# Performance work log

Measured on AMD Instinct MI355X. Metric: run time of the kernel, lower is better.

## Reference

```python
import jax, jax.numpy as jnp
import numpy as np

B, S, DIN = 4, 2048, 1024
H, D = 16, 64  # num_head, per-head dim_out


def _xavier(key, shape):
    fan_in, fan_out = shape[0], shape[1]
    limit = float(np.sqrt(6.0 / (fan_in + fan_out)))
    return jax.random.uniform(key, shape, jnp.float32, -limit, limit)


def setup_inputs() -> dict:
    key = jax.random.key(0)
    k_x, k_q, k_k, k_v, k_o = jax.random.split(key, 5)
    inputs = jax.random.normal(k_x, (B, S, DIN), jnp.float32)
    # weights stored as [in, out] (transpose of torch Linear.weight); bias zeros
    return {
        "inputs": inputs,
        "wq": _xavier(k_q, (DIN, H * D)), "bq": jnp.zeros((H * D,), jnp.float32),
        "wk": _xavier(k_k, (DIN, H * D)), "bk": jnp.zeros((H * D,), jnp.float32),
        "wv": _xavier(k_v, (DIN, H * D)), "bv": jnp.zeros((H * D,), jnp.float32),
        "wo": _xavier(k_o, (H * D, D)),  "bo": jnp.zeros((D,), jnp.float32),
    }


def reference(inputs, wq, bq, wk, bk, wv, bv, wo, bo):
    b, s, _ = inputs.shape
    q = (inputs @ wq + bq).reshape(b, s, H, D).transpose(0, 2, 1, 3)  # bhsd
    k = (inputs @ wk + bk).reshape(b, s, H, D).transpose(0, 2, 1, 3)
    v = (inputs @ wv + bv).reshape(b, s, H, D).transpose(0, 2, 1, 3)
    scores = jnp.einsum('bhsd,bhSd->bhsS', q, k) / jnp.sqrt(jnp.float32(D))
    p = jax.nn.softmax(scores, axis=-1)
    o = jnp.einsum('bhsS,bhSd->bhsd', p, v)
    o = o.transpose(0, 2, 1, 3).reshape(b, s, H * D)
    return o @ wo + bo  # [b, s, D]
```

## Files before the change

### kernel.cpp

```cpp
#include <hip/hip_runtime.h>

typedef __attribute__((ext_vector_type(8))) __bf16 bf16x8;
typedef __attribute__((ext_vector_type(4))) float f32x4;

#define NB   4
#define NS   2048
#define NDIN 1024
#define NH   16
#define ND   64
#define NHD  1024
#define NM   (NB * NS)

__device__ __forceinline__ float bf2f(unsigned short u) {
    unsigned int x = ((unsigned int)u) << 16;
    return __builtin_bit_cast(float, x);
}
__device__ __forceinline__ unsigned short f2bf(float f) {
    unsigned int u = __builtin_bit_cast(unsigned int, f);
    u += 0x7fff + ((u >> 16) & 1);
    return (unsigned short)(u >> 16);
}
__device__ __forceinline__ unsigned int cvt_pk_bf16(float lo, float hi) {
    unsigned int r;
    asm("v_cvt_pk_bf16_f32 %0, %1, %2" : "=v"(r) : "v"(lo), "v"(hi));
    return r;
}
__device__ __forceinline__ void gload16(const unsigned short* g, unsigned short* l) {
    __builtin_amdgcn_global_load_lds((const __attribute__((address_space(1))) unsigned int*)g,
                                     (__attribute__((address_space(3))) unsigned int*)l, 16, 0, 0);
}

__global__ __launch_bounds__(256) void cvt_x(const float* __restrict__ src,
                                             unsigned short* __restrict__ dst) {
    int i = blockIdx.x * 256 + threadIdx.x;
    float4 a = ((const float4*)src)[i * 2];
    float4 b = ((const float4*)src)[i * 2 + 1];
    union { uint4 u; unsigned short s[8]; } o;
    o.s[0] = f2bf(a.x); o.s[1] = f2bf(a.y); o.s[2] = f2bf(a.z); o.s[3] = f2bf(a.w);
    o.s[4] = f2bf(b.x); o.s[5] = f2bf(b.y); o.s[6] = f2bf(b.z); o.s[7] = f2bf(b.w);
    *(uint4*)(dst + (size_t)i * 8) = o.u;
}

__global__ void transpose_cvt3(const float* __restrict__ wq, const float* __restrict__ wk,
                               const float* __restrict__ wv, unsigned short* __restrict__ dst_all) {
    __shared__ unsigned short t[32][33];
    const float* src = blockIdx.z == 0 ? wq : blockIdx.z == 1 ? wk : wv;
    unsigned short* dst = dst_all + (size_t)blockIdx.z * 1024 * 1024;
    int k0 = blockIdx.x * 32, n0 = blockIdx.y * 32;
    int tx = threadIdx.x, ty = threadIdx.y;
#pragma unroll
    for (int i = 0; i < 32; i += 8)
        t[ty + i][tx] = f2bf(src[(size_t)(k0 + ty + i) * 1024 + (n0 + tx)]);
    __syncthreads();
#pragma unroll
    for (int i = 0; i < 32; i += 8)
        dst[(size_t)(n0 + ty + i) * 1024 + (k0 + tx)] = t[tx][ty + i];
}

__global__ void transpose_cvt(const float* __restrict__ src,
                              unsigned short* __restrict__ dst, int K, int N) {
    __shared__ unsigned short t[32][33];
    int k0 = blockIdx.x * 32, n0 = blockIdx.y * 32;
    int tx = threadIdx.x, ty = threadIdx.y;
#pragma unroll
    for (int i = 0; i < 32; i += 8)
        t[ty + i][tx] = f2bf(src[(size_t)(k0 + ty + i) * N + (n0 + tx)]);
    __syncthreads();
#pragma unroll
    for (int i = 0; i < 32; i += 8)
        dst[(size_t)(n0 + ty + i) * K + (k0 + tx)] = t[tx][ty + i];
}

__global__ __launch_bounds__(256) void gemm_qkv(
    const unsigned short* __restrict__ X, const unsigned short* __restrict__ Wt,
    const float* __restrict__ bq, const float* __restrict__ bk,
    const float* __restrict__ bv,
    unsigned short* __restrict__ Q, unsigned short* __restrict__ K,
    unsigned short* __restrict__ V) {
    __shared__ unsigned short smem[128 * 128];
    unsigned short (*Al)[32] = (unsigned short (*)[32])smem;
    unsigned short (*Bl)[32] = (unsigned short (*)[32])(smem + 128 * 32);
    unsigned short (*Cl)[128] = (unsigned short (*)[128])smem;

    int lin = blockIdx.x;
    int xcd = lin & 7, ii = lin >> 3;
    int mt = xcd * 8 + (ii & 7);
    int nt = ii >> 3;
    int mb = mt * 128, nb = nt * 128;

    int tid = threadIdx.x;
    int wid = tid >> 6, lane = tid & 63, quad = lane >> 4, l16 = lane & 15;
    int wm = (wid & 1) * 64, wn = (wid >> 1) * 64;

    int srow = 16 * wid + (lane >> 2);
    int scol = (lane & 3) * 8;
    const unsigned short* pa0 = X + (size_t)(mb + srow) * NDIN + scol;
    const unsigned short* pa1 = pa0 + (size_t)64 * NDIN;
    const unsigned short* pb0 = Wt + (size_t)(nb + srow) * NDIN + scol;
    const unsigned short* pb1 = pb0 + (size_t)64 * NDIN;
    unsigned short* la = smem + wid * 512;
    unsigned short* lb = smem + 128 * 32 + wid * 512;

    f32x4 acc[4][4];
#pragma unroll
    for (int i = 0; i < 4; i++)
#pragma unroll
        for (int j = 0; j < 4; j++) acc[i][j] = (f32x4){0.f, 0.f, 0.f, 0.f};

    for (int k0 = 0; k0 < NDIN; k0 += 32) {
        gload16(pa0, la);
        gload16(pa1, la + 2048);
        gload16(pb0, lb);
        gload16(pb1, lb + 2048);
        pa0 += 32; pa1 += 32; pb0 += 32; pb1 += 32;
        __syncthreads();
        bf16x8 af[4], bfr[4];
#pragma unroll
        for (int i = 0; i < 4; i++)
            af[i] = *(const bf16x8*)(&Al[wm + i * 16 + l16][quad * 8]);
#pragma unroll
        for (int j = 0; j < 4; j++)
            bfr[j] = *(const bf16x8*)(&Bl[wn + j * 16 + l16][quad * 8]);
#pragma unroll
        for (int i = 0; i < 4; i++)
#pragma unroll
            for (int j = 0; j < 4; j++)
                acc[i][j] = __builtin_amdgcn_mfma_f32_16x16x32_bf16(af[i], bfr[j], acc[i][j], 0, 0, 0);
        __syncthreads();
    }

    int wsel = nb >> 10;
    const float* bias = (wsel == 0) ? bq : (wsel == 1) ? bk : bv;
    unsigned short* dstp = (wsel == 0) ? Q : (wsel == 1) ? K : V;
#pragma unroll
    for (int i = 0; i < 4; i++)
#pragma unroll
        for (int j = 0; j < 4; j++) {
            int nl = wn + j * 16 + l16;
            float bias_v = bias[(nb & 1023) + nl];
#pragma unroll
            for (int r = 0; r < 4; r++) {
                int ml = wm + i * 16 + quad * 4 + r;
                int pc = ((nl >> 3) ^ (ml & 15));
                Cl[ml][(pc << 3) | (nl & 7)] = f2bf(acc[i][j][r] + bias_v);
            }
        }
    __syncthreads();
    {
        int hl = tid >> 7, sl = tid & 127;
        int h = ((nb & 1023) >> 6) + hl;
        int m = mb + sl, b = m >> 11, sidx = m & 2047;
        unsigned short* orow = dstp + ((size_t)((b * NH + h) * NS + sidx)) * ND;
#pragma unroll
        for (int c = 0; c < 8; c++) {
            int pc = ((hl * 8 + c) ^ (sl & 15));
            *(uint4*)(orow + c * 8) = *(const uint4*)(&Cl[sl][pc << 3]);
        }
    }
}

__global__ __launch_bounds__(256) void attn(
    const unsigned short* __restrict__ Q, const unsigned short* __restrict__ K,
    const unsigned short* __restrict__ V, unsigned short* __restrict__ Obuf) {
    __shared__ unsigned short Kl[2][64][64];
    __shared__ unsigned short Vt[2][64][64];

    int lin = blockIdx.x;
    int xcd = lin & 7, idx = lin >> 3;
    int bh = ((idx >> 4) << 3) | xcd;
    int qt = idx & 15;

    size_t base = (size_t)bh * NS * ND;
    int tid = threadIdx.x, wid = tid >> 6, lane = tid & 63;
    int quad = lane >> 4, l16 = lane & 15;
    int lx = l16 & 7;
    int q0 = qt * 128 + wid * 32;

    bf16x8 qa[2][2];
#pragma unroll
    for (int s = 0; s < 2; s++)
#pragma unroll
        for (int f = 0; f < 2; f++) {
            union { uint4 u; unsigned short sv[8]; } in_, out_;
            in_.u = *(const uint4*)(Q + base + (size_t)(q0 + s * 16 + l16) * ND + f * 32 + quad * 8);
#pragma unroll
            for (int j = 0; j < 8; j++) out_.sv[j] = f2bf(bf2f(in_.sv[j]) * 0.125f);
            qa[s][f] = __builtin_bit_cast(bf16x8, out_.u);
        }

    float lrow[2] = {0.f, 0.f};
    f32x4 o[2][4];
#pragma unroll
    for (int s = 0; s < 2; s++)
#pragma unroll
        for (int t = 0; t < 4; t++) o[s][t] = (f32x4){0.f, 0.f, 0.f, 0.f};

    int c0 = tid, c1 = tid + 256;
    int kr0w = c0 >> 3, kc0 = c0 & 7, kg0c = kc0 ^ (kr0w & 7);
    int kr1w = c1 >> 3, kc1 = c1 & 7, kg1c = kc1 ^ (kr1w & 7);
    const unsigned short* kp0 = K + base + (size_t)kr0w * ND + kc0 * 8;
    const unsigned short* kp1 = K + base + (size_t)kr1w * ND + kc1 * 8;
    int p = tid & 31, dqA = tid >> 5, dqB = dqA + 8;
    int cp = ((p >> 4) << 2) | ((p >> 1) & 3);
    int ps = (((p >> 3) & 1) << 2) | ((p & 1) << 1);
    int cb = cp ^ ((dqA & 1) << 2);
    const unsigned short* vg = V + base + (size_t)(2 * p) * ND + dqA * 4;

    uint4 k0r, k1r;
    uint2 va0, va1, va2, va3;

    auto writeKV = [&](int buf) {
        *(uint4*)(&Kl[buf][kr0w][kg0c * 8]) = k0r;
        *(uint4*)(&Kl[buf][kr1w][kg1c * 8]) = k1r;
        unsigned short* vt = &Vt[buf][0][0];
        unsigned int w0 = __builtin_amdgcn_perm(va1.x, va0.x, 0x05040100u);
        unsigned int w1 = __builtin_amdgcn_perm(va1.x, va0.x, 0x07060302u);
        unsigned int w2 = __builtin_amdgcn_perm(va1.y, va0.y, 0x05040100u);
        unsigned int w3 = __builtin_amdgcn_perm(va1.y, va0.y, 0x07060302u);
        *(unsigned int*)(vt + (dqA * 4 + 0) * 64 + ((cb ^ 0) << 3) + ps) = w0;
        *(unsigned int*)(vt + (dqA * 4 + 1) * 64 + ((cb ^ 1) << 3) + ps) = w1;
        *(unsigned int*)(vt + (dqA * 4 + 2) * 64 + ((cb ^ 2) << 3) + ps) = w2;
        *(unsigned int*)(vt + (dqA * 4 + 3) * 64 + ((cb ^ 3) << 3) + ps) = w3;
        unsigned int x0 = __builtin_amdgcn_perm(va3.x, va2.x, 0x05040100u);
        unsigned int x1 = __builtin_amdgcn_perm(va3.x, va2.x, 0x07060302u);
        unsigned int x2 = __builtin_amdgcn_perm(va3.y, va2.y, 0x05040100u);
        unsigned int x3 = __builtin_amdgcn_perm(va3.y, va2.y, 0x07060302u);
        *(unsigned int*)(vt + (dqB * 4 + 0) * 64 + ((cb ^ 0) << 3) + ps) = x0;
        *(unsigned int*)(vt + (dqB * 4 + 1) * 64 + ((cb ^ 1) << 3) + ps) = x1;
        *(unsigned int*)(vt + (dqB * 4 + 2) * 64 + ((cb ^ 2) << 3) + ps) = x2;
        *(unsigned int*)(vt + (dqB * 4 + 3) * 64 + ((cb ^ 3) << 3) + ps) = x3;
    };

    k0r = *(const uint4*)kp0;
    k1r = *(const uint4*)kp1;
    va0 = *(const uint2*)(vg);
    va1 = *(const uint2*)(vg + ND);
    va2 = *(const uint2*)(vg + 32);
    va3 = *(const uint2*)(vg + ND + 32);
    writeKV(0);
    __syncthreads();

    int cur = 0;
    for (int kc = 0; kc < NS; kc += 64) {
        bool more = (kc + 64 < NS);
        if (more) {
            kp0 += 64 * ND; kp1 += 64 * ND; vg += 64 * ND;
            k0r = *(const uint4*)kp0;
            k1r = *(const uint4*)kp1;
            va0 = *(const uint2*)(vg);
            va1 = *(const uint2*)(vg + ND);
            va2 = *(const uint2*)(vg + 32);
            va3 = *(const uint2*)(vg + ND + 32);
        }

        const unsigned short (*Kc)[64] = Kl[cur];
        const unsigned short (*Vc)[64] = Vt[cur];

        f32x4 st[2][4];
        __builtin_amdgcn_s_setprio(1);
#pragma unroll
        for (int sub = 0; sub < 4; sub++) {
            bf16x8 kb0 = *(const bf16x8*)(&Kc[sub * 16 + l16][((quad ^ lx) << 3)]);
            bf16x8 kb1 = *(const bf16x8*)(&Kc[sub * 16 + l16][(((4 + quad) ^ lx) << 3)]);
#pragma unroll
            for (int s = 0; s < 2; s++) {
                f32x4 c = (f32x4){0.f, 0.f, 0.f, 0.f};
                c = __builtin_amdgcn_mfma_f32_16x16x32_bf16(kb0, qa[s][0], c, 0, 0, 0);
                c = __builtin_amdgcn_mfma_f32_16x16x32_bf16(kb1, qa[s][1], c, 0, 0, 0);
                st[s][sub] = c;
            }
        }
        __builtin_amdgcn_s_setprio(0);

        bf16x8 pb[2][2];
#pragma unroll
        for (int s = 0; s < 2; s++) {
            float sum = 0.f;
#pragma unroll
            for (int sub = 0; sub < 4; sub++)
#pragma unroll
                for (int r = 0; r < 4; r++) {
                    float pv = __expf(st[s][sub][r]);
                    st[s][sub][r] = pv;
                    sum += pv;
                }
            lrow[s] += sum;
            unsigned int a0 = cvt_pk_bf16(st[s][0][0], st[s][0][1]);
            unsigned int a1 = cvt_pk_bf16(st[s][0][2], st[s][0][3]);
            unsigned int a2 = cvt_pk_bf16(st[s][1][0], st[s][1][1]);
            unsigned int a3 = cvt_pk_bf16(st[s][1][2], st[s][1][3]);
            pb[s][0] = __builtin_bit_cast(bf16x8, (uint4){a0, a1, a2, a3});
            unsigned int b0 = cvt_pk_bf16(st[s][2][0], st[s][2][1]);
            unsigned int b1 = cvt_pk_bf16(st[s][2][2], st[s][2][3]);
            unsigned int b2 = cvt_pk_bf16(st[s][3][0], st[s][3][1]);
            unsigned int b3 = cvt_pk_bf16(st[s][3][2], st[s][3][3]);
            pb[s][1] = __builtin_bit_cast(bf16x8, (uint4){b0, b1, b2, b3});
        }

        __builtin_amdgcn_s_setprio(1);
#pragma unroll
        for (int t = 0; t < 4; t++) {
            bf16x8 vb0 = *(const bf16x8*)(&Vc[t * 16 + l16][((quad ^ lx) << 3)]);
            bf16x8 vb1 = *(const bf16x8*)(&Vc[t * 16 + l16][(((4 + quad) ^ lx) << 3)]);
#pragma unroll
            for (int s = 0; s < 2; s++) {
                o[s][t] = __builtin_amdgcn_mfma_f32_16x16x32_bf16(vb0, pb[s][0], o[s][t], 0, 0, 0);
                o[s][t] = __builtin_amdgcn_mfma_f32_16x16x32_bf16(vb1, pb[s][1], o[s][t], 0, 0, 0);
            }
        }
        __builtin_amdgcn_s_setprio(0);

        if (more) {
            int nxt = cur ^ 1;
            writeKV(nxt);
            __syncthreads();
            cur = nxt;
        }
    }

    int b = bh >> 4, h = bh & 15;
#pragma unroll
    for (int s = 0; s < 2; s++) {
        float ls = lrow[s];
        ls += __shfl_xor(ls, 16, 64);
        ls += __shfl_xor(ls, 32, 64);
        float inv = 1.0f / ls;
        int q = q0 + s * 16 + l16;
#pragma unroll
        for (int t = 0; t < 4; t++) {
            uint2 w;
            w.x = cvt_pk_bf16(o[s][t][0] * inv, o[s][t][1] * inv);
            w.y = cvt_pk_bf16(o[s][t][2] * inv, o[s][t][3] * inv);
            *(uint2*)(Obuf + (size_t)(b * NS + q) * NHD + h * ND + t * 16 + quad * 4) = w;
        }
    }
}

__global__ __launch_bounds__(256) void out_proj(
    const unsigned short* __restrict__ Obuf, const unsigned short* __restrict__ WoT,
    const float* __restrict__ bo, float* __restrict__ Out) {
    __shared__ float red[4][16][64];
    int m0 = blockIdx.x * 16;
    int tid = threadIdx.x, wid = tid >> 6, lane = tid & 63;
    int quad = lane >> 4, l16 = lane & 15;
    f32x4 acc[4];
#pragma unroll
    for (int t = 0; t < 4; t++) acc[t] = (f32x4){0.f, 0.f, 0.f, 0.f};
    int kb = wid * 256;
    for (int k0 = kb; k0 < kb + 256; k0 += 32) {
        bf16x8 a = *(const bf16x8*)(Obuf + (size_t)(m0 + l16) * NHD + k0 + quad * 8);
#pragma unroll
        for (int t = 0; t < 4; t++) {
            bf16x8 b = *(const bf16x8*)(WoT + (size_t)(t * 16 + l16) * NHD + k0 + quad * 8);
            acc[t] = __builtin_amdgcn_mfma_f32_16x16x32_bf16(a, b, acc[t], 0, 0, 0);
        }
    }
#pragma unroll
    for (int t = 0; t < 4; t++)
#pragma unroll
        for (int r = 0; r < 4; r++) red[wid][t * 4 + r][lane] = acc[t][r];
    __syncthreads();
    if (tid < 64) {
        int q2 = tid >> 4, s16 = tid & 15;
#pragma unroll
        for (int t = 0; t < 4; t++) {
            int n = t * 16 + s16;
            float bb = bo[n];
#pragma unroll
            for (int r = 0; r < 4; r++) {
                int idx = t * 4 + r;
                float v = red[0][idx][tid] + red[1][idx][tid] + red[2][idx][tid] + red[3][idx][tid];
                int m = m0 + q2 * 4 + r;
                Out[(size_t)m * ND + n] = v + bb;
            }
        }
    }
}

extern "C" void kernel_launch(void* const* d_in, const int* in_sizes, int n_in,
                              void* d_out, int out_size, void* d_ws, size_t ws_size,
                              hipStream_t stream) {
    const float* X  = (const float*)d_in[0];
    const float* wq = (const float*)d_in[1];
    const float* bq = (const float*)d_in[2];
    const float* wk = (const float*)d_in[3];
    const float* bk = (const float*)d_in[4];
    const float* wv = (const float*)d_in[5];
    const float* bv = (const float*)d_in[6];
    const float* wo = (const float*)d_in[7];
    const float* bo = (const float*)d_in[8];
    float* Out = (float*)d_out;

    char* w = (char*)d_ws;
    unsigned short* Wt  = (unsigned short*)w; w += (size_t)3072 * 1024 * 2;
    unsigned short* WoT = (unsigned short*)w; w += (size_t)64 * 1024 * 2;
    unsigned short* Xb  = (unsigned short*)w; w += (size_t)NM * NDIN * 2;
    unsigned short* Qb  = (unsigned short*)w; w += (size_t)NM * NHD * 2;
    unsigned short* Kb  = (unsigned short*)w; w += (size_t)NM * NHD * 2;
    unsigned short* Vb  = (unsigned short*)w; w += (size_t)NM * NHD * 2;
    unsigned short* Ob  = (unsigned short*)w; w += (size_t)NM * NHD * 2;

    cvt_x<<<NM * NDIN / (256 * 8), 256, 0, stream>>>(X, Xb);

    dim3 tb(32, 8);
    transpose_cvt3<<<dim3(32, 32, 3), tb, 0, stream>>>(wq, wk, wv, Wt);
    transpose_cvt<<<dim3(32, 2), tb, 0, stream>>>(wo, WoT, 1024, 64);

    gemm_qkv<<<1536, 256, 0, stream>>>(Xb, Wt, bq, bk, bv, Qb, Kb, Vb);
    attn<<<1024, 256, 0, stream>>>(Qb, Kb, Vb, Ob);
    out_proj<<<512, 256, 0, stream>>>(Ob, WoT, bo, Out);
}
```

Baseline: 277.4 us.

## Double-buffer QKV GEMM LDS tiles and split attention across eight waves

```diff
diff --git a/kernel.cpp b/kernel.cpp
--- a/kernel.cpp
+++ b/kernel.cpp
@@ -77,10 +77,7 @@
     const float* __restrict__ bv,
     unsigned short* __restrict__ Q, unsigned short* __restrict__ K,
     unsigned short* __restrict__ V) {
-    __shared__ unsigned short smem[128 * 128];
-    unsigned short (*Al)[32] = (unsigned short (*)[32])smem;
-    unsigned short (*Bl)[32] = (unsigned short (*)[32])(smem + 128 * 32);
-    unsigned short (*Cl)[128] = (unsigned short (*)[128])smem;
+    __shared__ unsigned short smem[16384];
 
     int lin = blockIdx.x;
     int xcd = lin & 7, ii = lin >> 3;
@@ -98,37 +95,47 @@
     const unsigned short* pa1 = pa0 + (size_t)64 * NDIN;
     const unsigned short* pb0 = Wt + (size_t)(nb + srow) * NDIN + scol;
     const unsigned short* pb1 = pb0 + (size_t)64 * NDIN;
-    unsigned short* la = smem + wid * 512;
-    unsigned short* lb = smem + 128 * 32 + wid * 512;
-
-    f32x4 acc[4][4];
-#pragma unroll
-    for (int i = 0; i < 4; i++)
-#pragma unroll
-        for (int j = 0; j < 4; j++) acc[i][j] = (f32x4){0.f, 0.f, 0.f, 0.f};
-
-    for (int k0 = 0; k0 < NDIN; k0 += 32) {
+
+    auto stage = [&](int buf) {
+        unsigned short* la = smem + buf * 8192 + wid * 512;
+        unsigned short* lb = smem + buf * 8192 + 4096 + wid * 512;
         gload16(pa0, la);
         gload16(pa1, la + 2048);
         gload16(pb0, lb);
         gload16(pb1, lb + 2048);
         pa0 += 32; pa1 += 32; pb0 += 32; pb1 += 32;
-        __syncthreads();
+    };
+
+    f32x4 acc[4][4];
+#pragma unroll
+    for (int i = 0; i < 4; i++)
+#pragma unroll
+        for (int j = 0; j < 4; j++) acc[i][j] = (f32x4){0.f, 0.f, 0.f, 0.f};
+
+    stage(0);
+    __syncthreads();
+    int cur = 0;
+    for (int k0 = 0; k0 < NDIN; k0 += 32) {
+        if (k0 + 32 < NDIN) stage(cur ^ 1);
+        const unsigned short* Ab = smem + cur * 8192;
+        const unsigned short* Bb = Ab + 4096;
         bf16x8 af[4], bfr[4];
 #pragma unroll
         for (int i = 0; i < 4; i++)
-            af[i] = *(const bf16x8*)(&Al[wm + i * 16 + l16][quad * 8]);
+            af[i] = *(const bf16x8*)(Ab + (wm + i * 16 + l16) * 32 + quad * 8);
 #pragma unroll
         for (int j = 0; j < 4; j++)
-            bfr[j] = *(const bf16x8*)(&Bl[wn + j * 16 + l16][quad * 8]);
+            bfr[j] = *(const bf16x8*)(Bb + (wn + j * 16 + l16) * 32 + quad * 8);
 #pragma unroll
         for (int i = 0; i < 4; i++)
 #pragma unroll
             for (int j = 0; j < 4; j++)
                 acc[i][j] = __builtin_amdgcn_mfma_f32_16x16x32_bf16(af[i], bfr[j], acc[i][j], 0, 0, 0);
         __syncthreads();
-    }
-
+        cur ^= 1;
+    }
+
+    unsigned short (*Cl)[128] = (unsigned short (*)[128])smem;
     int wsel = nb >> 10;
     const float* bias = (wsel == 0) ? bq : (wsel == 1) ? bk : bv;
     unsigned short* dstp = (wsel == 0) ? Q : (wsel == 1) ? K : V;
@@ -159,7 +166,7 @@
     }
 }
 
-__global__ __launch_bounds__(256) void attn(
+__global__ __launch_bounds__(512) void attn(
     const unsigned short* __restrict__ Q, const unsigned short* __restrict__ K,
     const unsigned short* __restrict__ V, unsigned short* __restrict__ Obuf) {
     __shared__ unsigned short Kl[2][64][64];
@@ -174,69 +181,50 @@
     int tid = threadIdx.x, wid = tid >> 6, lane = tid & 63;
     int quad = lane >> 4, l16 = lane & 15;
     int lx = l16 & 7;
-    int q0 = qt * 128 + wid * 32;
-
-    bf16x8 qa[2][2];
-#pragma unroll
-    for (int s = 0; s < 2; s++)
-#pragma unroll
-        for (int f = 0; f < 2; f++) {
-            union { uint4 u; unsigned short sv[8]; } in_, out_;
-            in_.u = *(const uint4*)(Q + base + (size_t)(q0 + s * 16 + l16) * ND + f * 32 + quad * 8);
-#pragma unroll
-            for (int j = 0; j < 8; j++) out_.sv[j] = f2bf(bf2f(in_.sv[j]) * 0.125f);
-            qa[s][f] = __builtin_bit_cast(bf16x8, out_.u);
-        }
-
-    float lrow[2] = {0.f, 0.f};
-    f32x4 o[2][4];
-#pragma unroll
-    for (int s = 0; s < 2; s++)
-#pragma unroll
-        for (int t = 0; t < 4; t++) o[s][t] = (f32x4){0.f, 0.f, 0.f, 0.f};
-
-    int c0 = tid, c1 = tid + 256;
-    int kr0w = c0 >> 3, kc0 = c0 & 7, kg0c = kc0 ^ (kr0w & 7);
-    int kr1w = c1 >> 3, kc1 = c1 & 7, kg1c = kc1 ^ (kr1w & 7);
-    const unsigned short* kp0 = K + base + (size_t)kr0w * ND + kc0 * 8;
-    const unsigned short* kp1 = K + base + (size_t)kr1w * ND + kc1 * 8;
-    int p = tid & 31, dqA = tid >> 5, dqB = dqA + 8;
+    int q0 = qt * 128 + wid * 16;
+
+    bf16x8 qa[2];
+#pragma unroll
+    for (int f = 0; f < 2; f++) {
+        union { uint4 u; unsigned short sv[8]; } in_, out_;
+        in_.u = *(const uint4*)(Q + base + (size_t)(q0 + l16) * ND + f * 32 + quad * 8);
+#pragma unroll
+        for (int j = 0; j < 8; j++) out_.sv[j] = f2bf(bf2f(in_.sv[j]) * 0.125f);
+        qa[f] = __builtin_bit_cast(bf16x8, out_.u);
+    }
+
+    float lrow = 0.f;
+    f32x4 o[4];
+#pragma unroll
+    for (int t = 0; t < 4; t++) o[t] = (f32x4){0.f, 0.f, 0.f, 0.f};
+
+    int krow = tid >> 3, kch = tid & 7, kgc = kch ^ (krow & 7);
+    const unsigned short* kp = K + base + (size_t)krow * ND + kch * 8;
+    int p = tid & 31, dq = tid >> 5;
     int cp = ((p >> 4) << 2) | ((p >> 1) & 3);
     int ps = (((p >> 3) & 1) << 2) | ((p & 1) << 1);
-    int cb = cp ^ ((dqA & 1) << 2);
-    const unsigned short* vg = V + base + (size_t)(2 * p) * ND + dqA * 4;
-
-    uint4 k0r, k1r;
-    uint2 va0, va1, va2, va3;
+    int cb = cp ^ ((dq & 1) << 2);
+    const unsigned short* vg = V + base + (size_t)(2 * p) * ND + dq * 4;
+
+    uint4 kreg;
+    uint2 va0, va1;
 
     auto writeKV = [&](int buf) {
-        *(uint4*)(&Kl[buf][kr0w][kg0c * 8]) = k0r;
-        *(uint4*)(&Kl[buf][kr1w][kg1c * 8]) = k1r;
+        *(uint4*)(&Kl[buf][krow][kgc * 8]) = kreg;
         unsigned short* vt = &Vt[buf][0][0];
         unsigned int w0 = __builtin_amdgcn_perm(va1.x, va0.x, 0x05040100u);
         unsigned int w1 = __builtin_amdgcn_perm(va1.x, va0.x, 0x07060302u);
         unsigned int w2 = __builtin_amdgcn_perm(va1.y, va0.y, 0x05040100u);
         unsigned int w3 = __builtin_amdgcn_perm(va1.y, va0.y, 0x07060302u);
-        *(unsigned int*)(vt + (dqA * 4 + 0) * 64 + ((cb ^ 0) << 3) + ps) = w0;
-        *(unsigned int*)(vt + (dqA * 4 + 1) * 64 + ((cb ^ 1) << 3) + ps) = w1;
-        *(unsigned int*)(vt + (dqA * 4 + 2) * 64 + ((cb ^ 2) << 3) + ps) = w2;
-        *(unsigned int*)(vt + (dqA * 4 + 3) * 64 + ((cb ^ 3) << 3) + ps) = w3;
-        unsigned int x0 = __builtin_amdgcn_perm(va3.x, va2.x, 0x05040100u);
-        unsigned int x1 = __builtin_amdgcn_perm(va3.x, va2.x, 0x07060302u);
-        unsigned int x2 = __builtin_amdgcn_perm(va3.y, va2.y, 0x05040100u);
-        unsigned int x3 = __builtin_amdgcn_perm(va3.y, va2.y, 0x07060302u);
-        *(unsigned int*)(vt + (dqB * 4 + 0) * 64 + ((cb ^ 0) << 3) + ps) = x0;
-        *(unsigned int*)(vt + (dqB * 4 + 1) * 64 + ((cb ^ 1) << 3) + ps) = x1;
-        *(unsigned int*)(vt + (dqB * 4 + 2) * 64 + ((cb ^ 2) << 3) + ps) = x2;
-        *(unsigned int*)(vt + (dqB * 4 + 3) * 64 + ((cb ^ 3) << 3) + ps) = x3;
+        *(unsigned int*)(vt + (dq * 4 + 0) * 64 + ((cb ^ 0) << 3) + ps) = w0;
+        *(unsigned int*)(vt + (dq * 4 + 1) * 64 + ((cb ^ 1) << 3) + ps) = w1;
+        *(unsigned int*)(vt + (dq * 4 + 2) * 64 + ((cb ^ 2) << 3) + ps) = w2;
+        *(unsigned int*)(vt + (dq * 4 + 3) * 64 + ((cb ^ 3) << 3) + ps) = w3;
     };
 
-    k0r = *(const uint4*)kp0;
-    k1r = *(const uint4*)kp1;
+    kreg = *(const uint4*)kp;
     va0 = *(const uint2*)(vg);
     va1 = *(const uint2*)(vg + ND);
-    va2 = *(const uint2*)(vg + 32);
-    va3 = *(const uint2*)(vg + ND + 32);
     writeKV(0);
     __syncthreads();
 
@@ -244,57 +232,50 @@
     for (int kc = 0; kc < NS; kc += 64) {
         bool more = (kc + 64 < NS);
         if (more) {
-            kp0 += 64 * ND; kp1 += 64 * ND; vg += 64 * ND;
-            k0r = *(const uint4*)kp0;
-            k1r = *(const uint4*)kp1;
+            kp += 64 * ND; vg += 64 * ND;
+            kreg = *(const uint4*)kp;
             va0 = *(const uint2*)(vg);
             va1 = *(const uint2*)(vg + ND);
-            va2 = *(const uint2*)(vg + 32);
-            va3 = *(const uint2*)(vg + ND + 32);
         }
 
         const unsigned short (*Kc)[64] = Kl[cur];
         const unsigned short (*Vc)[64] = Vt[cur];
 
-        f32x4 st[2][4];
+        f32x4 st[4];
         __builtin_amdgcn_s_setprio(1);
 #pragma unroll
         for (int sub = 0; sub < 4; sub++) {
             bf16x8 kb0 = *(const bf16x8*)(&Kc[sub * 16 + l16][((quad ^ lx) << 3)]);
             bf16x8 kb1 = *(const bf16x8*)(&Kc[sub * 16 + l16][(((4 + quad) ^ lx) << 3)]);
-#pragma unroll
-            for (int s = 0; s < 2; s++) {
-                f32x4 c = (f32x4){0.f, 0.f, 0.f, 0.f};
-                c = __builtin_amdgcn_mfma_f32_16x16x32_bf16(kb0, qa[s][0], c, 0, 0, 0);
-                c = __builtin_amdgcn_mfma_f32_16x16x32_bf16(kb1, qa[s][1], c, 0, 0, 0);
-                st[s][sub] = c;
-            }
+            f32x4 c = (f32x4){0.f, 0.f, 0.f, 0.f};
+            c = __builtin_amdgcn_mfma_f32_16x16x32_bf16(kb0, qa[0], c, 0, 0, 0);
+            c = __builtin_amdgcn_mfma_f32_16x16x32_bf16(kb1, qa[1], c, 0, 0, 0);
+            st[sub] = c;
         }
         __builtin_amdgcn_s_setprio(0);
 
-        bf16x8 pb[2][2];
-#pragma unroll
-        for (int s = 0; s < 2; s++) {
+        bf16x8 pb[2];
+        {
             float sum = 0.f;
 #pragma unroll
             for (int sub = 0; sub < 4; sub++)
 #pragma unroll
                 for (int r = 0; r < 4; r++) {
-                    float pv = __expf(st[s][sub][r]);
-                    st[s][sub][r] = pv;
+                    float pv = __expf(st[sub][r]);
+                    st[sub][r] = pv;
                     sum += pv;
                 }
-            lrow[s] += sum;
-            unsigned int a0 = cvt_pk_bf16(st[s][0][0], st[s][0][1]);
-            unsigned int a1 = cvt_pk_bf16(st[s][0][2], st[s][0][3]);
-            unsigned int a2 = cvt_pk_bf16(st[s][1][0], st[s][1][1]);
-            unsigned int a3 = cvt_pk_bf16(st[s][1][2], st[s][1][3]);
-            pb[s][0] = __builtin_bit_cast(bf16x8, (uint4){a0, a1, a2, a3});
-            unsigned int b0 = cvt_pk_bf16(st[s][2][0], st[s][2][1]);
-            unsigned int b1 = cvt_pk_bf16(st[s][2][2], st[s][2][3]);
-            unsigned int b2 = cvt_pk_bf16(st[s][3][0], st[s][3][1]);
-            unsigned int b3 = cvt_pk_bf16(st[s][3][2], st[s][3][3]);
-            pb[s][1] = __builtin_bit_cast(bf16x8, (uint4){b0, b1, b2, b3});
+            lrow += sum;
+            unsigned int a0 = cvt_pk_bf16(st[0][0], st[0][1]);
+            unsigned int a1 = cvt_pk_bf16(st[0][2], st[0][3]);
+            unsigned int a2 = cvt_pk_bf16(st[1][0], st[1][1]);
+            unsigned int a3 = cvt_pk_bf16(st[1][2], st[1][3]);
+            pb[0] = __builtin_bit_cast(bf16x8, (uint4){a0, a1, a2, a3});
+            unsigned int b0 = cvt_pk_bf16(st[2][0], st[2][1]);
+            unsigned int b1 = cvt_pk_bf16(st[2][2], st[2][3]);
+            unsigned int b2 = cvt_pk_bf16(st[3][0], st[3][1]);
+            unsigned int b3 = cvt_pk_bf16(st[3][2], st[3][3]);
+            pb[1] = __builtin_bit_cast(bf16x8, (uint4){b0, b1, b2, b3});
         }
 
         __builtin_amdgcn_s_setprio(1);
@@ -302,11 +283,8 @@
         for (int t = 0; t < 4; t++) {
             bf16x8 vb0 = *(const bf16x8*)(&Vc[t * 16 + l16][((quad ^ lx) << 3)]);
             bf16x8 vb1 = *(const bf16x8*)(&Vc[t * 16 + l16][(((4 + quad) ^ lx) << 3)]);
-#pragma unroll
-            for (int s = 0; s < 2; s++) {
-                o[s][t] = __builtin_amdgcn_mfma_f32_16x16x32_bf16(vb0, pb[s][0], o[s][t], 0, 0, 0);
-                o[s][t] = __builtin_amdgcn_mfma_f32_16x16x32_bf16(vb1, pb[s][1], o[s][t], 0, 0, 0);
-            }
+            o[t] = __builtin_amdgcn_mfma_f32_16x16x32_bf16(vb0, pb[0], o[t], 0, 0, 0);
+            o[t] = __builtin_amdgcn_mfma_f32_16x16x32_bf16(vb1, pb[1], o[t], 0, 0, 0);
         }
         __builtin_amdgcn_s_setprio(0);
 
@@ -319,18 +297,17 @@
     }
 
     int b = bh >> 4, h = bh & 15;
-#pragma unroll
-    for (int s = 0; s < 2; s++) {
-        float ls = lrow[s];
+    {
+        float ls = lrow;
         ls += __shfl_xor(ls, 16, 64);
         ls += __shfl_xor(ls, 32, 64);
         float inv = 1.0f / ls;
-        int q = q0 + s * 16 + l16;
+        int q = q0 + l16;
 #pragma unroll
         for (int t = 0; t < 4; t++) {
             uint2 w;
-            w.x = cvt_pk_bf16(o[s][t][0] * inv, o[s][t][1] * inv);
-            w.y = cvt_pk_bf16(o[s][t][2] * inv, o[s][t][3] * inv);
+            w.x = cvt_pk_bf16(o[t][0] * inv, o[t][1] * inv);
+            w.y = cvt_pk_bf16(o[t][2] * inv, o[t][3] * inv);
             *(uint2*)(Obuf + (size_t)(b * NS + q) * NHD + h * ND + t * 16 + quad * 4) = w;
         }
     }
@@ -407,6 +384,6 @@
     transpose_cvt<<<dim3(32, 2), tb, 0, stream>>>(wo, WoT, 1024, 64);
 
     gemm_qkv<<<1536, 256, 0, stream>>>(Xb, Wt, bq, bk, bv, Qb, Kb, Vb);
-    attn<<<1024, 256, 0, stream>>>(Qb, Kb, Vb, Ob);
+    attn<<<1024, 512, 0, stream>>>(Qb, Kb, Vb, Ob);
     out_proj<<<512, 256, 0, stream>>>(Ob, WoT, bo, Out);
 }
```

Result: faster. 266.1 us (-4.1%).

## Double-buffer QKV GEMM LDS tiles and widen attention blocks to 512 threads

Applied to the files above, without the earlier changes.

```diff
diff --git a/kernel.cpp b/kernel.cpp
--- a/kernel.cpp
+++ b/kernel.cpp
@@ -77,10 +77,7 @@
     const float* __restrict__ bv,
     unsigned short* __restrict__ Q, unsigned short* __restrict__ K,
     unsigned short* __restrict__ V) {
-    __shared__ unsigned short smem[128 * 128];
-    unsigned short (*Al)[32] = (unsigned short (*)[32])smem;
-    unsigned short (*Bl)[32] = (unsigned short (*)[32])(smem + 128 * 32);
-    unsigned short (*Cl)[128] = (unsigned short (*)[128])smem;
+    __shared__ unsigned short smem[16384];
 
     int lin = blockIdx.x;
     int xcd = lin & 7, ii = lin >> 3;
@@ -98,37 +95,47 @@
     const unsigned short* pa1 = pa0 + (size_t)64 * NDIN;
     const unsigned short* pb0 = Wt + (size_t)(nb + srow) * NDIN + scol;
     const unsigned short* pb1 = pb0 + (size_t)64 * NDIN;
-    unsigned short* la = smem + wid * 512;
-    unsigned short* lb = smem + 128 * 32 + wid * 512;
-
-    f32x4 acc[4][4];
-#pragma unroll
-    for (int i = 0; i < 4; i++)
-#pragma unroll
-        for (int j = 0; j < 4; j++) acc[i][j] = (f32x4){0.f, 0.f, 0.f, 0.f};
-
-    for (int k0 = 0; k0 < NDIN; k0 += 32) {
+
+    auto stage = [&](int buf) {
+        unsigned short* la = smem + buf * 8192 + wid * 512;
+        unsigned short* lb = smem + buf * 8192 + 4096 + wid * 512;
         gload16(pa0, la);
         gload16(pa1, la + 2048);
         gload16(pb0, lb);
         gload16(pb1, lb + 2048);
         pa0 += 32; pa1 += 32; pb0 += 32; pb1 += 32;
-        __syncthreads();
+    };
+
+    f32x4 acc[4][4];
+#pragma unroll
+    for (int i = 0; i < 4; i++)
+#pragma unroll
+        for (int j = 0; j < 4; j++) acc[i][j] = (f32x4){0.f, 0.f, 0.f, 0.f};
+
+    stage(0);
+    __syncthreads();
+    int cur = 0;
+    for (int k0 = 0; k0 < NDIN; k0 += 32) {
+        if (k0 + 32 < NDIN) stage(cur ^ 1);
+        const unsigned short* Ab = smem + cur * 8192;
+        const unsigned short* Bb = Ab + 4096;
         bf16x8 af[4], bfr[4];
 #pragma unroll
         for (int i = 0; i < 4; i++)
-            af[i] = *(const bf16x8*)(&Al[wm + i * 16 + l16][quad * 8]);
+            af[i] = *(const bf16x8*)(Ab + (wm + i * 16 + l16) * 32 + quad * 8);
 #pragma unroll
         for (int j = 0; j < 4; j++)
-            bfr[j] = *(const bf16x8*)(&Bl[wn + j * 16 + l16][quad * 8]);
+            bfr[j] = *(const bf16x8*)(Bb + (wn + j * 16 + l16) * 32 + quad * 8);
 #pragma unroll
         for (int i = 0; i < 4; i++)
 #pragma unroll
             for (int j = 0; j < 4; j++)
                 acc[i][j] = __builtin_amdgcn_mfma_f32_16x16x32_bf16(af[i], bfr[j], acc[i][j], 0, 0, 0);
         __syncthreads();
-    }
-
+        cur ^= 1;
+    }
+
+    unsigned short (*Cl)[128] = (unsigned short (*)[128])smem;
     int wsel = nb >> 10;
     const float* bias = (wsel == 0) ? bq : (wsel == 1) ? bk : bv;
     unsigned short* dstp = (wsel == 0) ? Q : (wsel == 1) ? K : V;
@@ -159,7 +166,7 @@
     }
 }
 
-__global__ __launch_bounds__(256) void attn(
+__global__ __launch_bounds__(512) void attn(
     const unsigned short* __restrict__ Q, const unsigned short* __restrict__ K,
     const unsigned short* __restrict__ V, unsigned short* __restrict__ Obuf) {
     __shared__ unsigned short Kl[2][64][64];
@@ -167,14 +174,14 @@
 
     int lin = blockIdx.x;
     int xcd = lin & 7, idx = lin >> 3;
-    int bh = ((idx >> 4) << 3) | xcd;
-    int qt = idx & 15;
+    int bh = ((idx >> 3) << 3) | xcd;
+    int qt = idx & 7;
 
     size_t base = (size_t)bh * NS * ND;
     int tid = threadIdx.x, wid = tid >> 6, lane = tid & 63;
     int quad = lane >> 4, l16 = lane & 15;
     int lx = l16 & 7;
-    int q0 = qt * 128 + wid * 32;
+    int q0 = qt * 256 + wid * 32;
 
     bf16x8 qa[2][2];
 #pragma unroll
@@ -195,48 +202,33 @@
 #pragma unroll
         for (int t = 0; t < 4; t++) o[s][t] = (f32x4){0.f, 0.f, 0.f, 0.f};
 
-    int c0 = tid, c1 = tid + 256;
-    int kr0w = c0 >> 3, kc0 = c0 & 7, kg0c = kc0 ^ (kr0w & 7);
-    int kr1w = c1 >> 3, kc1 = c1 & 7, kg1c = kc1 ^ (kr1w & 7);
-    const unsigned short* kp0 = K + base + (size_t)kr0w * ND + kc0 * 8;
-    const unsigned short* kp1 = K + base + (size_t)kr1w * ND + kc1 * 8;
-    int p = tid & 31, dqA = tid >> 5, dqB = dqA + 8;
+    int krow = tid >> 3, kch = tid & 7, kgc = kch ^ (krow & 7);
+    const unsigned short* kp = K + base + (size_t)krow * ND + kch * 8;
+    int p = tid & 31, dq = tid >> 5;
     int cp = ((p >> 4) << 2) | ((p >> 1) & 3);
     int ps = (((p >> 3) & 1) << 2) | ((p & 1) << 1);
-    int cb = cp ^ ((dqA & 1) << 2);
-    const unsigned short* vg = V + base + (size_t)(2 * p) * ND + dqA * 4;
-
-    uint4 k0r, k1r;
-    uint2 va0, va1, va2, va3;
+    int cb = cp ^ ((dq & 1) << 2);
+    const unsigned short* vg = V + base + (size_t)(2 * p) * ND + dq * 4;
+
+    uint4 kreg;
+    uint2 va0, va1;
 
     auto writeKV = [&](int buf) {
-        *(uint4*)(&Kl[buf][kr0w][kg0c * 8]) = k0r;
-        *(uint4*)(&Kl[buf][kr1w][kg1c * 8]) = k1r;
+        *(uint4*)(&Kl[buf][krow][kgc * 8]) = kreg;
         unsigned short* vt = &Vt[buf][0][0];
         unsigned int w0 = __builtin_amdgcn_perm(va1.x, va0.x, 0x05040100u);
         unsigned int w1 = __builtin_amdgcn_perm(va1.x, va0.x, 0x07060302u);
         unsigned int w2 = __builtin_amdgcn_perm(va1.y, va0.y, 0x05040100u);
         unsigned int w3 = __builtin_amdgcn_perm(va1.y, va0.y, 0x07060302u);
-        *(unsigned int*)(vt + (dqA * 4 + 0) * 64 + ((cb ^ 0) << 3) + ps) = w0;
-        *(unsigned int*)(vt + (dqA * 4 + 1) * 64 + ((cb ^ 1) << 3) + ps) = w1;
-        *(unsigned int*)(vt + (dqA * 4 + 2) * 64 + ((cb ^ 2) << 3) + ps) = w2;
-        *(unsigned int*)(vt + (dqA * 4 + 3) * 64 + ((cb ^ 3) << 3) + ps) = w3;
-        unsigned int x0 = __builtin_amdgcn_perm(va3.x, va2.x, 0x05040100u);
-        unsigned int x1 = __builtin_amdgcn_perm(va3.x, va2.x, 0x07060302u);
-        unsigned int x2 = __builtin_amdgcn_perm(va3.y, va2.y, 0x05040100u);
-        unsigned int x3 = __builtin_amdgcn_perm(va3.y, va2.y, 0x07060302u);
-        *(unsigned int*)(vt + (dqB * 4 + 0) * 64 + ((cb ^ 0) << 3) + ps) = x0;
-        *(unsigned int*)(vt + (dqB * 4 + 1) * 64 + ((cb ^ 1) << 3) + ps) = x1;
-        *(unsigned int*)(vt + (dqB * 4 + 2) * 64 + ((cb ^ 2) << 3) + ps) = x2;
-        *(unsigned int*)(vt + (dqB * 4 + 3) * 64 + ((cb ^ 3) << 3) + ps) = x3;
+        *(unsigned int*)(vt + (dq * 4 + 0) * 64 + ((cb ^ 0) << 3) + ps) = w0;
+        *(unsigned int*)(vt + (dq * 4 + 1) * 64 + ((cb ^ 1) << 3) + ps) = w1;
+        *(unsigned int*)(vt + (dq * 4 + 2) * 64 + ((cb ^ 2) << 3) + ps) = w2;
+        *(unsigned int*)(vt + (dq * 4 + 3) * 64 + ((cb ^ 3) << 3) + ps) = w3;
     };
 
-    k0r = *(const uint4*)kp0;
-    k1r = *(const uint4*)kp1;
+    kreg = *(const uint4*)kp;
     va0 = *(const uint2*)(vg);
     va1 = *(const uint2*)(vg + ND);
-    va2 = *(const uint2*)(vg + 32);
-    va3 = *(const uint2*)(vg + ND + 32);
     writeKV(0);
     __syncthreads();
 
@@ -244,13 +236,10 @@
     for (int kc = 0; kc < NS; kc += 64) {
         bool more = (kc + 64 < NS);
         if (more) {
-            kp0 += 64 * ND; kp1 += 64 * ND; vg += 64 * ND;
-            k0r = *(const uint4*)kp0;
-            k1r = *(const uint4*)kp1;
+            kp += 64 * ND; vg += 64 * ND;
+            kreg = *(const uint4*)kp;
             va0 = *(const uint2*)(vg);
             va1 = *(const uint2*)(vg + ND);
-            va2 = *(const uint2*)(vg + 32);
-            va3 = *(const uint2*)(vg + ND + 32);
         }
 
         const unsigned short (*Kc)[64] = Kl[cur];
@@ -407,6 +396,6 @@
     transpose_cvt<<<dim3(32, 2), tb, 0, stream>>>(wo, WoT, 1024, 64);
 
     gemm_qkv<<<1536, 256, 0, stream>>>(Xb, Wt, bq, bk, bv, Qb, Kb, Vb);
-    attn<<<1024, 256, 0, stream>>>(Qb, Kb, Vb, Ob);
+    attn<<<512, 512, 0, stream>>>(Qb, Kb, Vb, Ob);
     out_proj<<<512, 256, 0, stream>>>(Ob, WoT, bo, Out);
 }
```

Result: faster. 265.5 us (-4.3%).
